# Performance work log

Measured on AMD Instinct MI355X. Metric: run time of the kernel, lower is better.

The kernel has to match this reference:

```python
import jax, jax.numpy as jnp
import numpy as np

B, S, D = 16, 2048, 2048  # S == D required for m_q + output broadcast in original code


def setup_inputs() -> dict:
    key = jax.random.key(0)
    ks = jax.random.split(key, 8)
    scale = 1.0 / np.sqrt(D)
    return {
        "hidden_list": jax.random.normal(ks[0], (B, S, D), dtype=jnp.float32),
        "m_q": jax.random.normal(ks[1], (D,), dtype=jnp.float32),
        "Wq": jax.random.normal(ks[2], (D, D), dtype=jnp.float32) * scale,
        "bq": jax.random.normal(ks[3], (D,), dtype=jnp.float32) * scale,
        "Wm": jax.random.normal(ks[4], (D, D), dtype=jnp.float32) * scale,
        "bm": jax.random.normal(ks[5], (D,), dtype=jnp.float32) * scale,
        "Wa": jax.random.normal(ks[6], (D, D), dtype=jnp.float32) * scale,
        "ba": jax.random.normal(ks[7], (D,), dtype=jnp.float32) * scale,
    }


def reference(hidden_list, m_q, Wq, bq, Wm, bm, Wa, ba):
    # hidden_list: [B, S, D]; m_q: [D]
    hq = jnp.tanh(jnp.einsum("bsd,ed->bse", hidden_list, Wq) + bq)      # [B,S,D]
    mq = jnp.tanh(Wm @ m_q + bm)                                        # [D]
    Sg = hq * mq                                                        # gated bilinear, [B,S,D]
    alpha = jax.nn.softmax(jnp.einsum("bsd,ed->bse", Sg, Wa) + ba, axis=-1)  # [B,S,D]
    output = jnp.sum(alpha * hidden_list, axis=-1)                      # [B,S]
    m_q_new = m_q + output                                              # broadcast [D]+[B,S] (S==D)
    return output, m_q_new
```

## Files before the change

### kernel.cpp

```cpp
#include <hip/hip_runtime.h>

typedef unsigned short u16;
typedef short bf16x8 __attribute__((ext_vector_type(8)));
typedef u16 u16x8 __attribute__((ext_vector_type(8)));
typedef float f32x4 __attribute__((ext_vector_type(4)));

__device__ __forceinline__ float bf2f(u16 u) {
    union { unsigned u; float f; } c; c.u = ((unsigned)u) << 16; return c.f;
}
__device__ __forceinline__ u16 f2bf(float f) {
    union { float f; unsigned u; } c; c.f = f;
    unsigned r = c.u + 0x7FFFu + ((c.u >> 16) & 1u);
    return (u16)(r >> 16);
}
__device__ __forceinline__ float tanh_fast(float x) {
    float e = __expf(2.0f * x);
    return 1.0f - 2.0f / (e + 1.0f);
}
__device__ __forceinline__ void gll16(const void* g, void* l) {
    __builtin_amdgcn_global_load_lds((const __attribute__((address_space(1))) void*)g,
                                     (__attribute__((address_space(3))) void*)l, 16, 0, 0);
}

#define BAR() do { __builtin_amdgcn_sched_barrier(0); __builtin_amdgcn_s_barrier(); \
                   __builtin_amdgcn_sched_barrier(0); } while (0)

__global__ __launch_bounds__(256) void cvt_f32_bf16(const float* __restrict__ src,
                                                    u16* __restrict__ dst, int n8) {
    int i = blockIdx.x * blockDim.x + threadIdx.x;
    int stride = gridDim.x * blockDim.x;
    for (; i < n8; i += stride) {
        const float4* s = (const float4*)(src + (size_t)i * 8);
        float4 a = s[0], b = s[1];
        u16x8 o;
        o[0] = f2bf(a.x); o[1] = f2bf(a.y); o[2] = f2bf(a.z); o[3] = f2bf(a.w);
        o[4] = f2bf(b.x); o[5] = f2bf(b.y); o[6] = f2bf(b.z); o[7] = f2bf(b.w);
        *(u16x8*)(dst + (size_t)i * 8) = o;
    }
}

__global__ __launch_bounds__(256) void mq_kernel(const float* __restrict__ Wm,
                                                 const float* __restrict__ q,
                                                 const float* __restrict__ bm,
                                                 float* __restrict__ mq, int D) {
    int w = threadIdx.x >> 6, l = threadIdx.x & 63;
    int e = blockIdx.x * 4 + w;
    const float* wp = Wm + (size_t)e * D;
    float s = 0.f;
    for (int j = 0; j < D; j += 256) {
        float4 wv = *(const float4*)(wp + j + l * 4);
        float4 qv = *(const float4*)(q + j + l * 4);
        s += wv.x * qv.x + wv.y * qv.y + wv.z * qv.z + wv.w * qv.w;
    }
    #pragma unroll
    for (int o = 32; o >= 1; o >>= 1) s += __shfl_xor(s, o);
    if (l == 0) mq[e] = tanh_fast(s + bm[e]);
}

template <int EPI>
__global__ __launch_bounds__(512, 2) void gemm8(const u16* __restrict__ A,
                                                const u16* __restrict__ B,
                                                const float* __restrict__ bias,
                                                const float* __restrict__ gate,
                                                u16* __restrict__ C,
                                                int M, int N, int K) {
    __shared__ u16 sh[65536];
    char* LDS = (char*)sh;
    const int K2 = K * 2;
    const int KT = K >> 6;

    const int tid = threadIdx.x;
    const int w = tid >> 6, l = tid & 63;
    const int wm = w >> 2, wn = w & 3;

    int orig = blockIdx.x + gridDim.x * blockIdx.y;
    int nwg = gridDim.x * gridDim.y;
    int id = ((nwg & 7) == 0) ? ((orig & 7) * (nwg >> 3) + (orig >> 3)) : orig;
    const int tileN = (id % gridDim.x) * 256;
    const int tileM = (id / gridDim.x) * 256;

    const int r0 = (w * 2) * 8 + (l >> 3);
    const int r1 = (w * 2 + 1) * 8 + (l >> 3);
    const int cc = ((l & 7) ^ (l >> 3)) << 4;
    const char* srcA0 = (const char*)A + (size_t)(tileM + r0) * K2 + cc;
    const char* srcA1 = (const char*)A + (size_t)(tileM + r1) * K2 + cc;
    const char* srcB0 = (const char*)B + (size_t)(tileN + r0) * K2 + cc;
    const char* srcB1 = (const char*)B + (size_t)(tileN + r1) * K2 + cc;
    const int ldc0 = (w * 2) * 1024, ldc1 = (w * 2 + 1) * 1024;

#define STG_A(tk, h) do { size_t go = (size_t)(tk) * 128 + (size_t)(h) * 128 * K2; \
    int sb = ((((tk) & 1) * 2 + (h)) * 16384); \
    gll16(srcA0 + go, LDS + sb + ldc0); gll16(srcA1 + go, LDS + sb + ldc1); } while (0)
#define STG_B(tk, h) do { size_t go = (size_t)(tk) * 128 + (size_t)(h) * 128 * K2; \
    int sb = 65536 + ((((tk) & 1) * 2 + (h)) * 16384); \
    gll16(srcB0 + go, LDS + sb + ldc0); gll16(srcB1 + go, LDS + sb + ldc1); } while (0)

    const int sw = l & 7;
    const int rowA = (wm * 64 + (l & 15)) * 128;
    const int rowB = (wn * 32 + (l & 15)) * 128;
    const int ck0 = (((l >> 4) ^ sw) << 4);
    const int ck1 = (((4 + (l >> 4)) ^ sw) << 4);
    const char* pA0 = LDS + rowA + ck0;
    const char* pA1 = LDS + rowA + ck1;
    const char* pB0 = LDS + 65536 + rowB + ck0;
    const char* pB1 = LDS + 65536 + rowB + ck1;

    f32x4 acc[2][4][2][2] = {};
    bf16x8 afA[4][2], afB[4][2], bb0[2][2], bb1[2][2];

    STG_A(0, 0); STG_B(0, 0); STG_A(0, 1); STG_B(0, 1);
    STG_A(1, 0); STG_B(1, 0);
    asm volatile("s_waitcnt vmcnt(4)" ::: "memory");
    BAR();
    #pragma unroll
    for (int fm = 0; fm < 4; ++fm) {
        afA[fm][0] = *(const bf16x8*)(pA0 + fm * 2048);
        afA[fm][1] = *(const bf16x8*)(pA1 + fm * 2048);
    }
    #pragma unroll
    for (int fn = 0; fn < 2; ++fn) {
        bb0[fn][0] = *(const bf16x8*)(pB0 + fn * 2048);
        bb0[fn][1] = *(const bf16x8*)(pB1 + fn * 2048);
    }

#define MFMA_CLUSTER(QM, QN, AF, BF)                                            \
    __builtin_amdgcn_s_setprio(1);                                              \
    _Pragma("unroll")                                                           \
    for (int fm = 0; fm < 4; ++fm)                                              \
        _Pragma("unroll")                                                       \
        for (int fn = 0; fn < 2; ++fn) {                                        \
            acc[QM][fm][QN][fn] = __builtin_amdgcn_mfma_f32_16x16x32_bf16(      \
                AF[fm][0], BF[fn][0], acc[QM][fm][QN][fn], 0, 0, 0);            \
            acc[QM][fm][QN][fn] = __builtin_amdgcn_mfma_f32_16x16x32_bf16(      \
                AF[fm][1], BF[fn][1], acc[QM][fm][QN][fn], 0, 0, 0);            \
        }                                                                       \
    __builtin_amdgcn_s_setprio(0);

#define ITER(t, P) do {                                                         \
    constexpr int S1 = (2 * (P) + 1) * 16384;                                   \
    constexpr int SN = (2 * (1 - (P))) * 16384;                                 \
              \
    if ((t) + 1 < KT) STG_A((t) + 1, 1);                                        \
    _Pragma("unroll")                                                           \
    for (int fn = 0; fn < 2; ++fn) {                                            \
        bb1[fn][0] = *(const bf16x8*)(pB0 + S1 + fn * 2048);                    \
        bb1[fn][1] = *(const bf16x8*)(pB1 + S1 + fn * 2048);                    \
    }                                                                           \
    MFMA_CLUSTER(0, 0, afA, bb0)                                                \
    BAR();                                                                      \
              \
    if ((t) + 1 < KT) STG_B((t) + 1, 1);                                        \
    _Pragma("unroll")                                                           \
    for (int fm = 0; fm < 4; ++fm) {                                            \
        afB[fm][0] = *(const bf16x8*)(pA0 + S1 + fm * 2048);                    \
        afB[fm][1] = *(const bf16x8*)(pA1 + S1 + fm * 2048);                    \
    }                                                                           \
    MFMA_CLUSTER(0, 1, afA, bb1)                                                \
    BAR();                                                                      \
              \
    if ((t) + 2 < KT) { STG_A((t) + 2, 0);                                      \
        asm volatile("s_waitcnt vmcnt(6)" ::: "memory"); }                      \
    else if ((t) + 1 < KT)                                                      \
        asm volatile("s_waitcnt vmcnt(4)" ::: "memory");                        \
    MFMA_CLUSTER(1, 0, afB, bb0)                                                \
    BAR();                                                                      \
                                          \
    if ((t) + 2 < KT) { STG_B((t) + 2, 0);                                      \
        asm volatile("s_waitcnt vmcnt(4)" ::: "memory"); }                      \
    else if ((t) + 1 < KT)                                                      \
        asm volatile("s_waitcnt vmcnt(0)" ::: "memory");                        \
    if ((t) + 1 < KT) {                                                         \
        _Pragma("unroll")                                                       \
        for (int fm = 0; fm < 4; ++fm) {                                        \
            afA[fm][0] = *(const bf16x8*)(pA0 + SN + fm * 2048);                \
            afA[fm][1] = *(const bf16x8*)(pA1 + SN + fm * 2048);                \
        }                                                                       \
        _Pragma("unroll")                                                       \
        for (int fn = 0; fn < 2; ++fn) {                                        \
            bb0[fn][0] = *(const bf16x8*)(pB0 + SN + fn * 2048);                \
            bb0[fn][1] = *(const bf16x8*)(pB1 + SN + fn * 2048);                \
        }                                                                       \
    }                                                                           \
    MFMA_CLUSTER(1, 1, afB, bb1)                                                \
    BAR();                                                                      \
} while (0)

    for (int tt = 0; tt < KT; tt += 2) {
        ITER(tt, 0);
        ITER(tt + 1, 1);
    }
#undef ITER
#undef MFMA_CLUSTER
#undef STG_A
#undef STG_B

    const int cr = (l >> 4) * 4;
    const int cl = l & 15;
    #pragma unroll
    for (int qn = 0; qn < 2; ++qn)
        #pragma unroll
        for (int fn = 0; fn < 2; ++fn) {
            const int col = tileN + qn * 128 + wn * 32 + fn * 16 + cl;
            const float bs = bias[col];
            float gt = 0.f;
            if (EPI == 0) gt = gate[col];
            #pragma unroll
            for (int qm = 0; qm < 2; ++qm)
                #pragma unroll
                for (int fm = 0; fm < 4; ++fm)
                    #pragma unroll
                    for (int r = 0; r < 4; ++r) {
                        const int row = tileM + qm * 128 + wm * 64 + fm * 16 + cr + r;
                        float v = acc[qm][fm][qn][fn][r] + bs;
                        if (EPI == 0) v = tanh_fast(v) * gt;
                        C[(size_t)row * N + col] = f2bf(v);
                    }
        }
}

__global__ __launch_bounds__(256) void softmax_out(const u16* __restrict__ logits,
                                                   const float* __restrict__ hidden,
                                                   const float* __restrict__ m_q,
                                                   float* __restrict__ out,
                                                   int D, int R) {
    const int r = blockIdx.x;
    const int t = threadIdx.x;
    const int w = t >> 6, l = t & 63;
    const u16* lp = logits + (size_t)r * D + t * 8;
    const float* hp = hidden + (size_t)r * D + t * 8;

    bf16x8 lv = *(const bf16x8*)lp;
    float lf[8];
    #pragma unroll
    for (int j = 0; j < 8; ++j) lf[j] = bf2f((u16)lv[j]);
    float4 h0 = *(const float4*)hp;
    float4 h1 = *(const float4*)(hp + 4);
    float hv[8] = {h0.x, h0.y, h0.z, h0.w, h1.x, h1.y, h1.z, h1.w};

    float m = lf[0];
    #pragma unroll
    for (int j = 1; j < 8; ++j) m = fmaxf(m, lf[j]);
    #pragma unroll
    for (int o = 32; o >= 1; o >>= 1) m = fmaxf(m, __shfl_xor(m, o));

    __shared__ float red[8];
    if (l == 0) red[w] = m;
    __syncthreads();
    m = fmaxf(fmaxf(red[0], red[1]), fmaxf(red[2], red[3]));
    __syncthreads();

    float se = 0.f, sh = 0.f;
    #pragma unroll
    for (int j = 0; j < 8; ++j) {
        float e = __expf(lf[j] - m);
        se += e;
        sh += e * hv[j];
    }
    #pragma unroll
    for (int o = 32; o >= 1; o >>= 1) { se += __shfl_xor(se, o); sh += __shfl_xor(sh, o); }
    if (l == 0) { red[w] = se; red[4 + w] = sh; }
    __syncthreads();
    if (t == 0) {
        float SE = red[0] + red[1] + red[2] + red[3];
        float SH = red[4] + red[5] + red[6] + red[7];
        float o = SH / SE;
        out[r] = o;
        out[R + r] = m_q[r & (D - 1)] + o;
    }
}

extern "C" void kernel_launch(void* const* d_in, const int* in_sizes, int n_in,
                              void* d_out, int out_size, void* d_ws, size_t ws_size,
                              hipStream_t stream) {
    const float* hidden = (const float*)d_in[0];
    const float* m_q    = (const float*)d_in[1];
    const float* Wq     = (const float*)d_in[2];
    const float* bq     = (const float*)d_in[3];
    const float* Wm     = (const float*)d_in[4];
    const float* bm     = (const float*)d_in[5];
    const float* Wa     = (const float*)d_in[6];
    const float* ba     = (const float*)d_in[7];
    float* out = (float*)d_out;

    const int D = 2048;
    const int M = 16 * 2048;

    char* ws = (char*)d_ws;
    size_t oH  = 0;
    size_t oS  = oH  + (size_t)M * D * 2;
    size_t oWq = oS  + (size_t)M * D * 2;
    size_t oWa = oWq + (size_t)D * D * 2;
    size_t oMq = oWa + (size_t)D * D * 2;
    size_t need = oMq + (size_t)D * sizeof(float);
    if (ws_size < need) return;

    u16* hbf    = (u16*)(ws + oH);
    u16* Sg     = (u16*)(ws + oS);
    u16* Wqb    = (u16*)(ws + oWq);
    u16* Wab    = (u16*)(ws + oWa);
    float* mq   = (float*)(ws + oMq);
    u16* logits = hbf;

    cvt_f32_bf16<<<4096, 256, 0, stream>>>(hidden, hbf, M * D / 8);
    cvt_f32_bf16<<<1024, 256, 0, stream>>>(Wq, Wqb, D * D / 8);
    cvt_f32_bf16<<<1024, 256, 0, stream>>>(Wa, Wab, D * D / 8);
    mq_kernel<<<D / 4, 256, 0, stream>>>(Wm, m_q, bm, mq, D);

    dim3 grid(D / 256, M / 256);
    gemm8<0><<<grid, 512, 0, stream>>>(hbf, Wqb, bq, mq, Sg, M, D, D);
    gemm8<1><<<grid, 512, 0, stream>>>(Sg, Wab, ba, nullptr, logits, M, D, D);

    softmax_out<<<M, 256, 0, stream>>>(logits, hidden, m_q, out, D, M);
}
```

Before: 655.5 us.

## Restructure GEMM K-loop schedule with LDS reads before barriers per cluster

Reorders the LDS-fragment reads and global-to-LDS stage issues in the double-buffered bf16 MFMA main loop. Each MFMA cluster is now preceded by its own barrier, with its fragment loads done up front. The vmcnt wait thresholds change to match the new issue order. The aim is to hide LDS read latency and global load waits differently, at the cost of twice as many barriers per iteration.

New measurement: 663.9 us. Within noise of the previous version (+1.3%).

```diff
diff --git a/kernel.cpp b/kernel.cpp
--- a/kernel.cpp
+++ b/kernel.cpp
@@ -108,20 +108,23 @@
     f32x4 acc[2][4][2][2] = {};
     bf16x8 afA[4][2], afB[4][2], bb0[2][2], bb1[2][2];
 
+#define RD_A(DST, SLOT)                                                         \
+    _Pragma("unroll")                                                           \
+    for (int fm = 0; fm < 4; ++fm) {                                            \
+        DST[fm][0] = *(const bf16x8*)(pA0 + (SLOT) + fm * 2048);                \
+        DST[fm][1] = *(const bf16x8*)(pA1 + (SLOT) + fm * 2048);                \
+    }
+#define RD_B(DST, SLOT)                                                         \
+    _Pragma("unroll")                                                           \
+    for (int fn = 0; fn < 2; ++fn) {                                            \
+        DST[fn][0] = *(const bf16x8*)(pB0 + (SLOT) + fn * 2048);                \
+        DST[fn][1] = *(const bf16x8*)(pB1 + (SLOT) + fn * 2048);                \
+    }
+
     STG_A(0, 0); STG_B(0, 0); STG_A(0, 1); STG_B(0, 1);
     STG_A(1, 0); STG_B(1, 0);
     asm volatile("s_waitcnt vmcnt(4)" ::: "memory");
     BAR();
-    #pragma unroll
-    for (int fm = 0; fm < 4; ++fm) {
-        afA[fm][0] = *(const bf16x8*)(pA0 + fm * 2048);
-        afA[fm][1] = *(const bf16x8*)(pA1 + fm * 2048);
-    }
-    #pragma unroll
-    for (int fn = 0; fn < 2; ++fn) {
-        bb0[fn][0] = *(const bf16x8*)(pB0 + fn * 2048);
-        bb0[fn][1] = *(const bf16x8*)(pB1 + fn * 2048);
-    }
 
 #define MFMA_CLUSTER(QM, QN, AF, BF)                                            \
     __builtin_amdgcn_s_setprio(1);                                              \
@@ -137,50 +140,36 @@
     __builtin_amdgcn_s_setprio(0);
 
 #define ITER(t, P) do {                                                         \
+    constexpr int S0 = (2 * (P)) * 16384;                                       \
     constexpr int S1 = (2 * (P) + 1) * 16384;                                   \
-    constexpr int SN = (2 * (1 - (P))) * 16384;                                 \
-              \
-    if ((t) + 1 < KT) STG_A((t) + 1, 1);                                        \
-    _Pragma("unroll")                                                           \
-    for (int fn = 0; fn < 2; ++fn) {                                            \
-        bb1[fn][0] = *(const bf16x8*)(pB0 + S1 + fn * 2048);                    \
-        bb1[fn][1] = *(const bf16x8*)(pB1 + S1 + fn * 2048);                    \
-    }                                                                           \
+          \
+    RD_A(afA, S0)                                                               \
+    RD_B(bb0, S0)                                                               \
+    if ((t) + 1 < KT) { STG_A((t) + 1, 1);                                      \
+        asm volatile("s_waitcnt vmcnt(6)" ::: "memory"); }                      \
+    else                                                                        \
+        asm volatile("s_waitcnt vmcnt(0)" ::: "memory");                        \
+    BAR();                                                                      \
     MFMA_CLUSTER(0, 0, afA, bb0)                                                \
     BAR();                                                                      \
-              \
+                                            \
+    RD_B(bb1, S1)                                                               \
     if ((t) + 1 < KT) STG_B((t) + 1, 1);                                        \
-    _Pragma("unroll")                                                           \
-    for (int fm = 0; fm < 4; ++fm) {                                            \
-        afB[fm][0] = *(const bf16x8*)(pA0 + S1 + fm * 2048);                    \
-        afB[fm][1] = *(const bf16x8*)(pA1 + S1 + fm * 2048);                    \
-    }                                                                           \
+    BAR();                                                                      \
     MFMA_CLUSTER(0, 1, afA, bb1)                                                \
     BAR();                                                                      \
-              \
-    if ((t) + 2 < KT) { STG_A((t) + 2, 0);                                      \
-        asm volatile("s_waitcnt vmcnt(6)" ::: "memory"); }                      \
+                                            \
+    RD_A(afB, S1)                                                               \
+    if ((t) + 2 < KT) STG_A((t) + 2, 0);                                        \
+    BAR();                                                                      \
+    MFMA_CLUSTER(1, 0, afB, bb0)                                                \
+    BAR();                                                                      \
+        \
+    if ((t) + 2 < KT) { STG_B((t) + 2, 0);                                      \
+        asm volatile("s_waitcnt vmcnt(8)" ::: "memory"); }                      \
     else if ((t) + 1 < KT)                                                      \
         asm volatile("s_waitcnt vmcnt(4)" ::: "memory");                        \
-    MFMA_CLUSTER(1, 0, afB, bb0)                                                \
-    BAR();                                                                      \
-                                          \
-    if ((t) + 2 < KT) { STG_B((t) + 2, 0);                                      \
-        asm volatile("s_waitcnt vmcnt(4)" ::: "memory"); }                      \
-    else if ((t) + 1 < KT)                                                      \
-        asm volatile("s_waitcnt vmcnt(0)" ::: "memory");                        \
-    if ((t) + 1 < KT) {                                                         \
-        _Pragma("unroll")                                                       \
-        for (int fm = 0; fm < 4; ++fm) {                                        \
-            afA[fm][0] = *(const bf16x8*)(pA0 + SN + fm * 2048);                \
-            afA[fm][1] = *(const bf16x8*)(pA1 + SN + fm * 2048);                \
-        }                                                                       \
-        _Pragma("unroll")                                                       \
-        for (int fn = 0; fn < 2; ++fn) {                                        \
-            bb0[fn][0] = *(const bf16x8*)(pB0 + SN + fn * 2048);                \
-            bb0[fn][1] = *(const bf16x8*)(pB1 + SN + fn * 2048);                \
-        }                                                                       \
-    }                                                                           \
+    BAR();                                                                      \
     MFMA_CLUSTER(1, 1, afB, bb1)                                                \
     BAR();                                                                      \
 } while (0)
@@ -191,6 +180,8 @@
     }
 #undef ITER
 #undef MFMA_CLUSTER
+#undef RD_A
+#undef RD_B
 #undef STG_A
 #undef STG_B
 
```
